# Kernel tuning notes

Hardware: AMD Instinct MI355X
Metric: run time of the kernel (lower is better)

Reference implementation:

```python
import jax, jax.numpy as jnp
import numpy as np

N = 100000      # nodes
E = 1600000     # edges (avg degree 16)
F_IN = 64       # num_features
HID = 16        # hidden channels (fixed in module)
OUT = 32        # num_classes
K = 2           # kernel_size (dim=1, degree=1 open B-spline -> 2 basis fns)


def setup_inputs() -> dict:
    key = jax.random.key(0)
    ks = jax.random.split(key, 8)
    return {
        "x": jax.random.normal(ks[0], (N, F_IN), jnp.float32),
        "edge_index": jax.random.randint(ks[1], (2, E), 0, N, dtype=jnp.int64),
        "dropout": 0,  # unused in eval mode (F.dropout training=False)
        "edge_attr": jnp.full((E, 1), 0.1, jnp.float32),  # nt([0.1]) broadcast per edge
        "W1": jax.random.normal(ks[2], (K, F_IN, HID), jnp.float32) / np.sqrt(K * F_IN).astype(np.float32),
        "root1": jax.random.normal(ks[3], (F_IN, HID), jnp.float32) / np.sqrt(F_IN).astype(np.float32),
        "bias1": jnp.zeros((HID,), jnp.float32),
        "W2": jax.random.normal(ks[4], (K, HID, OUT), jnp.float32) / np.sqrt(K * HID).astype(np.float32),
        "root2": jax.random.normal(ks[5], (HID, OUT), jnp.float32) / np.sqrt(HID).astype(np.float32),
        "bias2": jnp.zeros((OUT,), jnp.float32),
    }


def spline_conv(x, edge_index, edge_attr, W, root, bias):
    """SplineConv, dim=1, kernel_size=2, degree=1 open B-spline, aggr='mean'."""
    src, dst = edge_index[0], edge_index[1]
    n = x.shape[0]
    u = edge_attr[:, 0]                                  # [E] pseudo-coords in [0,1]
    # degree-1 open spline, kernel_size=2: frac = u*(ks-1) = u; kernels {0,1}
    basis = jnp.stack([1.0 - u, u], axis=1)              # [E, K]
    # transform at node level (cheaper than gathering raw features per edge)
    h = jnp.einsum('nf,kfo->nko', x, W)                  # [N, K, out]
    msg = jnp.einsum('ek,eko->eo', basis, h[src])        # [E, out]
    summed = jax.ops.segment_sum(msg, dst, num_segments=n)
    deg = jax.ops.segment_sum(jnp.ones_like(u), dst, num_segments=n)
    out = summed / jnp.maximum(deg, 1.0)[:, None]        # mean aggregation
    return out + x @ root + bias                          # root weight + bias


def reference(x, edge_index, dropout, edge_attr, W1, root1, bias1, W2, root2, bias2):
    # dropout is a no-op in eval mode
    h = jax.nn.elu(spline_conv(x, edge_index, edge_attr, W1, root1, bias1))
    h = spline_conv(h, edge_index, edge_attr, W2, root2, bias2)
    return jax.nn.log_softmax(h, axis=1)
```

## Files before the change

### kernel.cpp

```cpp
#include <hip/hip_runtime.h>
#include <math.h>

#define NN 100000
#define NE 1600000
#define F_IN 64
#define HID 16
#define OUTF 32
#define BKT_SHIFT 6
#define BKT_NODES 64
#define NBKT 1563
#define SRCM 0x1FFFF
#define CAP_REG 2048
#define CAP_LDS 1536
#define PBLK2 512
#define EPB2 (NE / PBLK2)
#define OVF_MAX 4096

__device__ __forceinline__ unsigned bf16r(float f) {
    unsigned u = __float_as_uint(f);
    return (u + 0x7FFFu + ((u >> 16) & 1u)) >> 16;
}
__device__ __forceinline__ float bfa(unsigned p) { return __uint_as_float(p << 16); }
__device__ __forceinline__ float bfd(unsigned p) { return __uint_as_float(p & 0xFFFF0000u); }
__device__ __forceinline__ float bfh(unsigned short v) { return __uint_as_float(((unsigned)v) << 16); }

__global__ __launch_bounds__(1024) void partF_kernel(const int* __restrict__ ei,
                                                     const float* __restrict__ ea,
                                                     int* __restrict__ gcur,
                                                     int* __restrict__ novf,
                                                     int4* __restrict__ ovf,
                                                     int2* __restrict__ bkt) {
    __shared__ int hcnt[NBKT];
    __shared__ int hbase[NBKT];
    __shared__ int lbase[NBKT];
    __shared__ int s[1024];
    __shared__ int2 sbuf[EPB2];
    __shared__ unsigned short bid[EPB2];
    int t = threadIdx.x, blk = blockIdx.x;
    for (int i = t; i < NBKT; i += 1024) hcnt[i] = 0;
    __syncthreads();
    int beg = blk * EPB2, end = beg + EPB2;
    for (int e = beg + t; e < end; e += 1024)
        atomicAdd(&hcnt[ei[NE + e] >> BKT_SHIFT], 1);
    __syncthreads();
    int i0 = 2 * t, i1 = 2 * t + 1;
    int v0 = (i0 < NBKT) ? hcnt[i0] : 0;
    int v1 = (i1 < NBKT) ? hcnt[i1] : 0;
    s[t] = v0 + v1;
    __syncthreads();
    for (int off = 1; off < 1024; off <<= 1) {
        int xv = (t >= off) ? s[t - off] : 0;
        __syncthreads();
        s[t] += xv;
        __syncthreads();
    }
    int run = (t == 0) ? 0 : s[t - 1];
    if (i0 < NBKT) lbase[i0] = run;
    if (i1 < NBKT) lbase[i1] = run + v0;
    __syncthreads();
    for (int i = t; i < NBKT; i += 1024) {
        int c = hcnt[i];
        hbase[i] = c ? atomicAdd(&gcur[i], c) : 0;
        hcnt[i] = 0;
    }
    __syncthreads();
    for (int e = beg + t; e < end; e += 1024) {
        int src = ei[e];
        int dst = ei[NE + e];
        float u = ea[e];
        int b = dst >> BKT_SHIFT;
        int r = atomicAdd(&hcnt[b], 1);
        int lp = lbase[b] + r;
        sbuf[lp] = make_int2(src | ((dst & (BKT_NODES - 1)) << 17), __float_as_int(u));
        bid[lp] = (unsigned short)b;
    }
    __syncthreads();
    for (int i = t; i < EPB2; i += 1024) {
        int2 pk = sbuf[i];
        int b = bid[i];
        int p = hbase[b] + (i - lbase[b]);
        if (p < CAP_REG) {
            bkt[(size_t)b * CAP_REG + p] = pk;
        } else {
            int o = atomicAdd(novf, 1);
            if (o < OVF_MAX)
                ovf[o] = make_int4(b * BKT_NODES + (pk.x >> 17), pk.x & SRCM, pk.y, 0);
        }
    }
}

__global__ __launch_bounds__(256) void proj1_kernel(const float* __restrict__ x,
                                                    const float* __restrict__ W1,
                                                    const float* __restrict__ root1,
                                                    const float* __restrict__ bias1,
                                                    unsigned* __restrict__ ab1p,
                                                    float* __restrict__ r1) {
    __shared__ float w[2 * F_IN * HID];
    __shared__ float wr[F_IN * HID];
    __shared__ float bb[HID];
    for (int i = threadIdx.x; i < 2 * F_IN * HID; i += 256) w[i] = W1[i];
    for (int i = threadIdx.x; i < F_IN * HID; i += 256) wr[i] = root1[i];
    if (threadIdx.x < HID) bb[threadIdx.x] = bias1[threadIdx.x];
    __syncthreads();
    int n = blockIdx.x * 256 + threadIdx.x;
    if (n >= NN) return;
    float accA[HID], accB[HID], accR[HID];
#pragma unroll
    for (int o = 0; o < HID; ++o) { accA[o] = 0.f; accB[o] = 0.f; accR[o] = bb[o]; }
    const float* xr = x + (size_t)n * F_IN;
    for (int f = 0; f < F_IN; ++f) {
        float xv = xr[f];
        const float* w0 = &w[f * HID];
        const float* w1 = &w[F_IN * HID + f * HID];
        const float* w2 = &wr[f * HID];
#pragma unroll
        for (int o = 0; o < HID; ++o) {
            accA[o] = fmaf(xv, w0[o], accA[o]);
            accB[o] = fmaf(xv, w1[o], accB[o]);
            accR[o] = fmaf(xv, w2[o], accR[o]);
        }
    }
    unsigned* ar = ab1p + (size_t)n * HID;
    float* rr = r1 + (size_t)n * HID;
#pragma unroll
    for (int o = 0; o < HID; ++o) {
        ar[o] = bf16r(accA[o]) | (bf16r(accB[o] - accA[o]) << 16);
        rr[o] = accR[o];
    }
}

__global__ __launch_bounds__(512) void gather1_kernel(const int* __restrict__ gcur,
                                                      const int* __restrict__ novf,
                                                      const int4* __restrict__ ovf,
                                                      int2* __restrict__ bkt,
                                                      const unsigned* __restrict__ ab1p,
                                                      const float* __restrict__ r1,
                                                      unsigned short* __restrict__ h16,
                                                      float* __restrict__ dinv,
                                                      int* __restrict__ segg) {
    __shared__ int2 sorted[CAP_LDS];
    __shared__ int cnt[BKT_NODES], cur[BKT_NODES], segb[BKT_NODES + 1];
    __shared__ float accL[BKT_NODES * HID];
    __shared__ float degsL[BKT_NODES];
    int t = threadIdx.x;
    int b = blockIdx.x;
    int tot = gcur[b];
    int beg = b * CAP_REG;
    if (t < BKT_NODES) { cnt[t] = 0; cur[t] = 0; degsL[t] = 0.f; }
    __syncthreads();
    int nodeBase = b * BKT_NODES;

    if (tot <= CAP_LDS) {
        int end = beg + tot;
        for (int e = beg + t; e < end; e += 512)
            atomicAdd(&cnt[((unsigned)bkt[e].x) >> 17], 1);
        __syncthreads();
        if (t < BKT_NODES) {
            int v = cnt[t];
            int sc = v;
#pragma unroll
            for (int off = 1; off < 64; off <<= 1) {
                int o = __shfl_up(sc, off, 64);
                if (t >= off) sc += o;
            }
            segb[t] = sc - v;
            if (t == 63) segb[64] = sc;
        }
        __syncthreads();
        for (int e = beg + t; e < end; e += 512) {
            int2 pk = bkt[e];
            int loc = ((unsigned)pk.x) >> 17;
            int pos = segb[loc] + atomicAdd(&cur[loc], 1);
            sorted[pos] = pk;
        }
        __syncthreads();
        for (int e = t; e < tot; e += 512) bkt[beg + e] = sorted[e];
        if (t <= BKT_NODES) segg[b * (BKT_NODES + 1) + t] = segb[t];
        int j = t & (HID - 1);
        int g = t >> 4;
        int s = segb[2 * g], mid = segb[2 * g + 1], e2 = segb[2 * g + 2];
        float a0 = 0.f, a1 = 0.f;
        int e = s;
        for (; e + 8 <= e2; e += 8) {
            float val[8]; int sel[8];
#pragma unroll
            for (int k = 0; k < 8; ++k) {
                int2 pk = sorted[e + k];
                unsigned p = ab1p[(size_t)(pk.x & SRCM) * HID + j];
                val[k] = fmaf(__int_as_float(pk.y), bfd(p), bfa(p));
                sel[k] = (e + k) >= mid;
            }
#pragma unroll
            for (int k = 0; k < 8; ++k) {
                a0 += sel[k] ? 0.f : val[k];
                a1 += sel[k] ? val[k] : 0.f;
            }
        }
        for (; e < e2; ++e) {
            int2 pk = sorted[e];
            unsigned p = ab1p[(size_t)(pk.x & SRCM) * HID + j];
            float val = fmaf(__int_as_float(pk.y), bfd(p), bfa(p));
            if (e >= mid) a1 += val; else a0 += val;
        }
        float d0 = 1.f / (float)max(mid - s, 1);
        float d1 = 1.f / (float)max(e2 - mid, 1);
        int n0 = nodeBase + 2 * g, n1 = n0 + 1;
        if (n0 < NN) {
            float v = a0 * d0 + r1[(size_t)n0 * HID + j];
            h16[(size_t)n0 * HID + j] = (unsigned short)bf16r(v > 0.f ? v : expm1f(v));
            if (j == 0) dinv[n0] = d0;
        }
        if (n1 < NN) {
            float v = a1 * d1 + r1[(size_t)n1 * HID + j];
            h16[(size_t)n1 * HID + j] = (unsigned short)bf16r(v > 0.f ? v : expm1f(v));
            if (j == 0) dinv[n1] = d1;
        }
    } else {
        int inreg = min(tot, CAP_REG);
        int end = beg + inreg;
        for (int i = t; i < BKT_NODES * HID; i += 512) accL[i] = 0.f;
        __syncthreads();
        int j = t & (HID - 1);
        int g = t >> 4;
        for (int e = beg + g; e < end; e += 32) {
            int2 pk = bkt[e];
            unsigned p = ab1p[(size_t)(pk.x & SRCM) * HID + j];
            atomicAdd(&accL[(((unsigned)pk.x) >> 17) * HID + j],
                      fmaf(__int_as_float(pk.y), bfd(p), bfa(p)));
            if (j == 0) atomicAdd(&degsL[((unsigned)pk.x) >> 17], 1.f);
        }
        int ovn = min(novf[0], OVF_MAX);
        for (int o = 0; o < ovn; ++o) {
            int4 ent = ovf[o];
            int loc = ent.x - nodeBase;
            if (loc >= 0 && loc < BKT_NODES && g == 0) {
                unsigned p = ab1p[(size_t)ent.y * HID + j];
                atomicAdd(&accL[loc * HID + j], fmaf(__int_as_float(ent.z), bfd(p), bfa(p)));
                if (j == 0) atomicAdd(&degsL[loc], 1.f);
            }
        }
        __syncthreads();
        if (t < BKT_NODES) degsL[t] = 1.f / fmaxf(degsL[t], 1.f);
        __syncthreads();
#pragma unroll
        for (int it = 0; it < BKT_NODES * HID / 512; ++it) {
            int idx = it * 512 + t;
            int nl = idx >> 4, jj = idx & (HID - 1);
            int n = nodeBase + nl;
            if (n < NN) {
                float v = accL[idx] * degsL[nl] + r1[(size_t)n * HID + jj];
                h16[(size_t)n * HID + jj] = (unsigned short)bf16r(v > 0.f ? v : expm1f(v));
            }
        }
        if (t < BKT_NODES && nodeBase + t < NN) dinv[nodeBase + t] = degsL[t];
    }
}

__global__ __launch_bounds__(512) void gather2_kernel(const int* __restrict__ gcur,
                                                      const int* __restrict__ novf,
                                                      const int4* __restrict__ ovf,
                                                      const int2* __restrict__ bkt,
                                                      const unsigned short* __restrict__ h16,
                                                      const float* __restrict__ W2,
                                                      const float* __restrict__ root2,
                                                      const float* __restrict__ bias2,
                                                      const float* __restrict__ dinv,
                                                      const int* __restrict__ segg,
                                                      float* __restrict__ out) {
    __shared__ int segb[BKT_NODES + 1];
    __shared__ float s0L[BKT_NODES * HID];
    __shared__ float s1L[BKT_NODES * HID];
    __shared__ float w20[HID * OUTF], w2d[HID * OUTF], wr[HID * OUTF];
    __shared__ float bb[OUTF];
    int t = threadIdx.x;
    for (int i = t; i < HID * OUTF; i += 512) {
        float a = W2[i];
        w20[i] = a;
        w2d[i] = W2[HID * OUTF + i] - a;
        wr[i] = root2[i];
    }
    if (t < OUTF) bb[t] = bias2[t];
    int b = blockIdx.x;
    int tot = gcur[b];
    int beg = b * CAP_REG;
    int nodeBase = b * BKT_NODES;
    if (t <= BKT_NODES) segb[t] = segg[b * (BKT_NODES + 1) + t];
    __syncthreads();

    if (tot <= CAP_LDS) {
        const int2* sp = bkt + beg;
        int j = t & (HID - 1);
        int g = t >> 4;
        int s = segb[2 * g], mid = segb[2 * g + 1], e2 = segb[2 * g + 2];
        float s00 = 0.f, s10 = 0.f, s01 = 0.f, s11 = 0.f;
        int e = s;
        for (; e + 8 <= e2; e += 8) {
            float hv[8], uv[8]; int sel[8];
#pragma unroll
            for (int k = 0; k < 8; ++k) {
                int2 pk = sp[e + k];
                hv[k] = bfh(h16[(size_t)(pk.x & SRCM) * HID + j]);
                uv[k] = __int_as_float(pk.y);
                sel[k] = (e + k) >= mid;
            }
#pragma unroll
            for (int k = 0; k < 8; ++k) {
                float uh = uv[k] * hv[k];
                s00 += sel[k] ? 0.f : hv[k];
                s10 += sel[k] ? 0.f : uh;
                s01 += sel[k] ? hv[k] : 0.f;
                s11 += sel[k] ? uh : 0.f;
            }
        }
        for (; e < e2; ++e) {
            int2 pk = sp[e];
            float hvv = bfh(h16[(size_t)(pk.x & SRCM) * HID + j]);
            float uh = __int_as_float(pk.y) * hvv;
            if (e >= mid) { s01 += hvv; s11 += uh; }
            else          { s00 += hvv; s10 += uh; }
        }
        s0L[(2 * g) * HID + j] = s00;
        s1L[(2 * g) * HID + j] = s10;
        s0L[(2 * g + 1) * HID + j] = s01;
        s1L[(2 * g + 1) * HID + j] = s11;
        __syncthreads();
    } else {
        int inreg = min(tot, CAP_REG);
        int end = beg + inreg;
        for (int i = t; i < BKT_NODES * HID; i += 512) { s0L[i] = 0.f; s1L[i] = 0.f; }
        __syncthreads();
        int j = t & (HID - 1);
        int g = t >> 4;
        for (int e = beg + g; e < end; e += 32) {
            int2 pk = bkt[e];
            float hvv = bfh(h16[(size_t)(pk.x & SRCM) * HID + j]);
            int l = ((unsigned)pk.x) >> 17;
            atomicAdd(&s0L[l * HID + j], hvv);
            atomicAdd(&s1L[l * HID + j], __int_as_float(pk.y) * hvv);
        }
        int ovn = min(novf[0], OVF_MAX);
        for (int o = 0; o < ovn; ++o) {
            int4 ent = ovf[o];
            int loc = ent.x - nodeBase;
            if (loc >= 0 && loc < BKT_NODES && g == 0) {
                float hvv = bfh(h16[(size_t)ent.y * HID + j]);
                atomicAdd(&s0L[loc * HID + j], hvv);
                atomicAdd(&s1L[loc * HID + j], __int_as_float(ent.z) * hvv);
            }
        }
        __syncthreads();
    }

#pragma unroll
    for (int it = 0; it < BKT_NODES * OUTF / 512; ++it) {
        int idx = it * 512 + t;
        int nl = idx >> 5, jj = idx & (OUTF - 1);
        int n = nodeBase + nl;
        float v = 0.f;
        if (n < NN) {
            float msum = 0.f;
            const float* S0 = &s0L[nl * HID];
            const float* S1 = &s1L[nl * HID];
#pragma unroll
            for (int f = 0; f < HID; ++f)
                msum += S0[f] * w20[f * OUTF + jj] + S1[f] * w2d[f * OUTF + jj];
            v = msum * dinv[n] + bb[jj];
            const unsigned short* hr = h16 + (size_t)n * HID;
#pragma unroll
            for (int f = 0; f < HID; ++f)
                v = fmaf(bfh(hr[f]), wr[f * OUTF + jj], v);
        }
        float m = v;
#pragma unroll
        for (int mask = 16; mask >= 1; mask >>= 1) m = fmaxf(m, __shfl_xor(m, mask));
        float ex = expf(v - m);
        float sm = ex;
#pragma unroll
        for (int mask = 16; mask >= 1; mask >>= 1) sm += __shfl_xor(sm, mask);
        if (n < NN) out[(size_t)n * OUTF + jj] = v - m - logf(sm);
    }
}

extern "C" void kernel_launch(void* const* d_in, const int* in_sizes, int n_in,
                              void* d_out, int out_size, void* d_ws, size_t ws_size,
                              hipStream_t stream) {
    const float* x     = (const float*)d_in[0];
    const int*   ei    = (const int*)d_in[1];
    const float* ea    = (const float*)d_in[3];
    const float* W1    = (const float*)d_in[4];
    const float* root1 = (const float*)d_in[5];
    const float* bias1 = (const float*)d_in[6];
    const float* W2    = (const float*)d_in[7];
    const float* root2 = (const float*)d_in[8];
    const float* bias2 = (const float*)d_in[9];
    float* out = (float*)d_out;
    float* ws  = (float*)d_ws;

    const size_t N = NN;
    int*            gcur = (int*)(ws);
    int*            novf = (int*)(ws + 2000);
    int4*           ovf  = (int4*)(ws + 2048);
    float*          dinv = ws + 20000;
    int*            segg = (int*)(ws + 120000);
    float*          r1   = ws + 222000;
    unsigned*       ab1p = (unsigned*)(ws + 222000 + 16 * N);
    unsigned short* h16  = (unsigned short*)(ws + 222000 + 32 * N);
    int2*           bkt  = (int2*)(ws + 222000 + 40 * N);

    hipMemsetAsync(gcur, 0, 8448, stream);

    int nbN = (NN + 255) / 256;
    partF_kernel<<<PBLK2, 1024, 0, stream>>>(ei, ea, gcur, novf, ovf, bkt);
    proj1_kernel<<<nbN, 256, 0, stream>>>(x, W1, root1, bias1, ab1p, r1);
    gather1_kernel<<<NBKT, 512, 0, stream>>>(gcur, novf, ovf, bkt, ab1p, r1, h16, dinv, segg);
    gather2_kernel<<<NBKT, 512, 0, stream>>>(gcur, novf, ovf, bkt, h16, W2, root2, bias2, dinv, segg, out);
}
```

Baseline: 138.1 us.

## Stage bucket edges in LDS, split per-node gather loops, replace memset kernel

Gather1 now copies each bucket's edges into shared memory once and reuses that copy for counting and scattering, instead of reading global memory twice. Gather2 also stages its bucket into shared memory. In both gathers the unrolled loop is split into separate passes for the two nodes each thread group handles, which removes the per-edge select logic. A tiny zeroing kernel replaces hipMemsetAsync, and gather1 writes a -1 sentinel into segg for overflow buckets so gather2 takes the atomic path for them. The cost is more LDS per block, which may lower occupancy.

```diff
diff --git a/kernel.cpp b/kernel.cpp
--- a/kernel.cpp
+++ b/kernel.cpp
@@ -24,6 +24,13 @@
 __device__ __forceinline__ float bfd(unsigned p) { return __uint_as_float(p & 0xFFFF0000u); }
 __device__ __forceinline__ float bfh(unsigned short v) { return __uint_as_float(((unsigned)v) << 16); }
 
+__global__ __launch_bounds__(256) void zeroG_kernel(int* __restrict__ gcur,
+                                                    int* __restrict__ novf) {
+    int t = blockIdx.x * 256 + threadIdx.x;
+    if (t < NBKT) gcur[t] = 0;
+    if (t == NBKT) novf[0] = 0;
+}
+
 __global__ __launch_bounds__(1024) void partF_kernel(const int* __restrict__ ei,
                                                      const float* __restrict__ ea,
                                                      int* __restrict__ gcur,
@@ -138,9 +145,9 @@
                                                       unsigned short* __restrict__ h16,
                                                       float* __restrict__ dinv,
                                                       int* __restrict__ segg) {
+    __shared__ int2 raw[CAP_LDS];
     __shared__ int2 sorted[CAP_LDS];
     __shared__ int cnt[BKT_NODES], cur[BKT_NODES], segb[BKT_NODES + 1];
-    __shared__ float accL[BKT_NODES * HID];
     __shared__ float degsL[BKT_NODES];
     int t = threadIdx.x;
     int b = blockIdx.x;
@@ -151,9 +158,10 @@
     int nodeBase = b * BKT_NODES;
 
     if (tot <= CAP_LDS) {
-        int end = beg + tot;
-        for (int e = beg + t; e < end; e += 512)
-            atomicAdd(&cnt[((unsigned)bkt[e].x) >> 17], 1);
+        for (int e = t; e < tot; e += 512) raw[e] = bkt[beg + e];
+        __syncthreads();
+        for (int e = t; e < tot; e += 512)
+            atomicAdd(&cnt[((unsigned)raw[e].x) >> 17], 1);
         __syncthreads();
         if (t < BKT_NODES) {
             int v = cnt[t];
@@ -167,8 +175,8 @@
             if (t == 63) segb[64] = sc;
         }
         __syncthreads();
-        for (int e = beg + t; e < end; e += 512) {
-            int2 pk = bkt[e];
+        for (int e = t; e < tot; e += 512) {
+            int2 pk = raw[e];
             int loc = ((unsigned)pk.x) >> 17;
             int pos = segb[loc] + atomicAdd(&cur[loc], 1);
             sorted[pos] = pk;
@@ -181,26 +189,37 @@
         int s = segb[2 * g], mid = segb[2 * g + 1], e2 = segb[2 * g + 2];
         float a0 = 0.f, a1 = 0.f;
         int e = s;
-        for (; e + 8 <= e2; e += 8) {
-            float val[8]; int sel[8];
+        for (; e + 8 <= mid; e += 8) {
+            float val[8];
 #pragma unroll
             for (int k = 0; k < 8; ++k) {
                 int2 pk = sorted[e + k];
                 unsigned p = ab1p[(size_t)(pk.x & SRCM) * HID + j];
                 val[k] = fmaf(__int_as_float(pk.y), bfd(p), bfa(p));
-                sel[k] = (e + k) >= mid;
-            }
-#pragma unroll
-            for (int k = 0; k < 8; ++k) {
-                a0 += sel[k] ? 0.f : val[k];
-                a1 += sel[k] ? val[k] : 0.f;
-            }
+            }
+#pragma unroll
+            for (int k = 0; k < 8; ++k) a0 += val[k];
+        }
+        for (; e < mid; ++e) {
+            int2 pk = sorted[e];
+            unsigned p = ab1p[(size_t)(pk.x & SRCM) * HID + j];
+            a0 += fmaf(__int_as_float(pk.y), bfd(p), bfa(p));
+        }
+        for (; e + 8 <= e2; e += 8) {
+            float val[8];
+#pragma unroll
+            for (int k = 0; k < 8; ++k) {
+                int2 pk = sorted[e + k];
+                unsigned p = ab1p[(size_t)(pk.x & SRCM) * HID + j];
+                val[k] = fmaf(__int_as_float(pk.y), bfd(p), bfa(p));
+            }
+#pragma unroll
+            for (int k = 0; k < 8; ++k) a1 += val[k];
         }
         for (; e < e2; ++e) {
             int2 pk = sorted[e];
             unsigned p = ab1p[(size_t)(pk.x & SRCM) * HID + j];
-            float val = fmaf(__int_as_float(pk.y), bfd(p), bfa(p));
-            if (e >= mid) a1 += val; else a0 += val;
+            a1 += fmaf(__int_as_float(pk.y), bfd(p), bfa(p));
         }
         float d0 = 1.f / (float)max(mid - s, 1);
         float d1 = 1.f / (float)max(e2 - mid, 1);
@@ -216,6 +235,7 @@
             if (j == 0) dinv[n1] = d1;
         }
     } else {
+        float* accL = (float*)raw;
         int inreg = min(tot, CAP_REG);
         int end = beg + inreg;
         for (int i = t; i < BKT_NODES * HID; i += 512) accL[i] = 0.f;
@@ -241,6 +261,7 @@
         }
         __syncthreads();
         if (t < BKT_NODES) degsL[t] = 1.f / fmaxf(degsL[t], 1.f);
+        if (t == 0) segg[b * (BKT_NODES + 1)] = -1;
         __syncthreads();
 #pragma unroll
         for (int it = 0; it < BKT_NODES * HID / 512; ++it) {
@@ -267,6 +288,7 @@
                                                       const float* __restrict__ dinv,
                                                       const int* __restrict__ segg,
                                                       float* __restrict__ out) {
+    __shared__ int2 sbufL[CAP_LDS];
     __shared__ int segb[BKT_NODES + 1];
     __shared__ float s0L[BKT_NODES * HID];
     __shared__ float s1L[BKT_NODES * HID];
@@ -287,37 +309,53 @@
     if (t <= BKT_NODES) segb[t] = segg[b * (BKT_NODES + 1) + t];
     __syncthreads();
 
-    if (tot <= CAP_LDS) {
-        const int2* sp = bkt + beg;
+    if (tot <= CAP_LDS && segb[0] != -1) {
+        for (int e = t; e < tot; e += 512) sbufL[e] = bkt[beg + e];
+        __syncthreads();
         int j = t & (HID - 1);
         int g = t >> 4;
         int s = segb[2 * g], mid = segb[2 * g + 1], e2 = segb[2 * g + 2];
         float s00 = 0.f, s10 = 0.f, s01 = 0.f, s11 = 0.f;
         int e = s;
-        for (; e + 8 <= e2; e += 8) {
-            float hv[8], uv[8]; int sel[8];
-#pragma unroll
-            for (int k = 0; k < 8; ++k) {
-                int2 pk = sp[e + k];
+        for (; e + 8 <= mid; e += 8) {
+            float hv[8], uv[8];
+#pragma unroll
+            for (int k = 0; k < 8; ++k) {
+                int2 pk = sbufL[e + k];
                 hv[k] = bfh(h16[(size_t)(pk.x & SRCM) * HID + j]);
                 uv[k] = __int_as_float(pk.y);
-                sel[k] = (e + k) >= mid;
-            }
-#pragma unroll
-            for (int k = 0; k < 8; ++k) {
-                float uh = uv[k] * hv[k];
-                s00 += sel[k] ? 0.f : hv[k];
-                s10 += sel[k] ? 0.f : uh;
-                s01 += sel[k] ? hv[k] : 0.f;
-                s11 += sel[k] ? uh : 0.f;
+            }
+#pragma unroll
+            for (int k = 0; k < 8; ++k) {
+                s00 += hv[k];
+                s10 = fmaf(uv[k], hv[k], s10);
+            }
+        }
+        for (; e < mid; ++e) {
+            int2 pk = sbufL[e];
+            float hvv = bfh(h16[(size_t)(pk.x & SRCM) * HID + j]);
+            s00 += hvv;
+            s10 = fmaf(__int_as_float(pk.y), hvv, s10);
+        }
+        for (; e + 8 <= e2; e += 8) {
+            float hv[8], uv[8];
+#pragma unroll
+            for (int k = 0; k < 8; ++k) {
+                int2 pk = sbufL[e + k];
+                hv[k] = bfh(h16[(size_t)(pk.x & SRCM) * HID + j]);
+                uv[k] = __int_as_float(pk.y);
+            }
+#pragma unroll
+            for (int k = 0; k < 8; ++k) {
+                s01 += hv[k];
+                s11 = fmaf(uv[k], hv[k], s11);
             }
         }
         for (; e < e2; ++e) {
-            int2 pk = sp[e];
+            int2 pk = sbufL[e];
             float hvv = bfh(h16[(size_t)(pk.x & SRCM) * HID + j]);
-            float uh = __int_as_float(pk.y) * hvv;
-            if (e >= mid) { s01 += hvv; s11 += uh; }
-            else          { s00 += hvv; s10 += uh; }
+            s01 += hvv;
+            s11 = fmaf(__int_as_float(pk.y), hvv, s11);
         }
         s0L[(2 * g) * HID + j] = s00;
         s1L[(2 * g) * HID + j] = s10;
@@ -407,9 +445,8 @@
     unsigned short* h16  = (unsigned short*)(ws + 222000 + 32 * N);
     int2*           bkt  = (int2*)(ws + 222000 + 40 * N);
 
-    hipMemsetAsync(gcur, 0, 8448, stream);
-
     int nbN = (NN + 255) / 256;
+    zeroG_kernel<<<(NBKT + 256) / 256, 256, 0, stream>>>(gcur, novf);
     partF_kernel<<<PBLK2, 1024, 0, stream>>>(ei, ea, gcur, novf, ovf, bkt);
     proj1_kernel<<<nbN, 256, 0, stream>>>(x, W1, root1, bias1, ab1p, r1);
     gather1_kernel<<<NBKT, 512, 0, stream>>>(gcur, novf, ovf, bkt, ab1p, r1, h16, dinv, segg);
```

Measured after the change: 127.3 us. 7.8% less time.
